# Optimization experiments

Hardware: AMD Instinct MI355X
Metric: run time of the kernel (lower is better)

## Reference

```python
import jax, jax.numpy as jnp
import numpy as np

N, L, C, H = 8, 2048, 512, 512
C_HALF = max(C // 2, 1)


def setup_inputs() -> dict:
    key = jax.random.key(0)
    ks = jax.random.split(key, 11)
    s = 0.02
    return {
        "x": jax.random.normal(ks[0], (N, L, C), dtype=jnp.float32),
        "theta_w": jax.random.normal(ks[1], (C, H), dtype=jnp.float32) * s,
        "theta_b": jax.random.normal(ks[2], (H,), dtype=jnp.float32) * s,
        "phi_w": jax.random.normal(ks[3], (C, H), dtype=jnp.float32) * s,
        "phi_b": jax.random.normal(ks[4], (H,), dtype=jnp.float32) * s,
        "psi_w": jax.random.normal(ks[5], (C, H), dtype=jnp.float32) * s,
        "psi_b": jax.random.normal(ks[6], (H,), dtype=jnp.float32) * s,
        "r1_w": jax.random.normal(ks[7], (H, C_HALF), dtype=jnp.float32) * s,
        "r1_b": jax.random.normal(ks[8], (C_HALF,), dtype=jnp.float32) * s,
        "r2_w": jax.random.normal(ks[9], (C_HALF, C), dtype=jnp.float32) * s,
        "r2_b": jax.random.normal(ks[10], (C,), dtype=jnp.float32) * s,
    }


def reference(x, theta_w, theta_b, phi_w, phi_b, psi_w, psi_b, r1_w, r1_b, r2_w, r2_b):
    # projections: [n, L, h]
    x_t = x @ theta_w + theta_b
    x_ph = x @ phi_w + phi_b
    x_psi = x @ psi_w + psi_b
    # unscaled attention: phi @ theta^T -> [n, L, L], softmax over last dim
    attn = jax.nn.softmax(jnp.einsum("nlh,nmh->nlm", x_ph, x_t), axis=2)
    x_add = jnp.einsum("nlm,nmh->nlh", attn, x_psi)
    # recover MLP with LeakyReLU(0.2) then Tanh, residual add
    h1 = jax.nn.leaky_relu(x_add @ r1_w + r1_b, negative_slope=0.2)
    h2 = jnp.tanh(h1 @ r2_w + r2_b)
    return x + h2
```

## Files before the change

kernel.cpp:

```cpp
#include <hip/hip_runtime.h>
#include <hip/hip_bf16.h>

typedef float f32x4 __attribute__((ext_vector_type(4)));
typedef int   v8i   __attribute__((ext_vector_type(8)));
typedef __attribute__((address_space(3))) unsigned int       lds_uint;
typedef __attribute__((address_space(1))) const unsigned int glb_uint;

__device__ __forceinline__ float tanh_fast(float x) {
    float e = __expf(-2.0f * fabsf(x));
    float r = (1.0f - e) / (1.0f + e);
    return copysignf(r, x);
}
__device__ __forceinline__ unsigned char f2fp8(float v) {
    return (unsigned char)(__builtin_amdgcn_cvt_pk_fp8_f32(v, 0.0f, 0, false) & 0xff);
}
__device__ __forceinline__ unsigned short f2h(float v) {
    _Float16 h = (_Float16)v;
    unsigned short u;
    __builtin_memcpy(&u, &h, 2);
    return u;
}
__device__ __forceinline__ float h2f(unsigned short u) {
    _Float16 h;
    __builtin_memcpy(&h, &u, 2);
    return (float)h;
}

__global__ __launch_bounds__(256) void prep(
    const float* __restrict__ x,
    const float* __restrict__ theta_w, const float* __restrict__ phi_w,
    const float* __restrict__ psi_w,   const float* __restrict__ r1_w,
    const float* __restrict__ r2_w,
    const float* __restrict__ theta_b, const float* __restrict__ phi_b,
    const float* __restrict__ psi_b,
    unsigned char* __restrict__ xb8, unsigned char* __restrict__ wCat8T,
    unsigned char* __restrict__ r1T8, unsigned char* __restrict__ r2T8,
    float* __restrict__ bCat) {
    const int b = blockIdx.x, t = threadIdx.x;
    if (b < 8192) {
        long i = ((long)b * 256 + t) * 4;
        float4 f = *(const float4*)(x + i);
        int w = __builtin_amdgcn_cvt_pk_fp8_f32(f.x, f.y, 0, false);
        w = __builtin_amdgcn_cvt_pk_fp8_f32(f.z, f.w, w, true);
        *(unsigned int*)(xb8 + i) = (unsigned int)w;
    } else if (b < 11264) {
        const int sel = (b - 8192) >> 10;
        const int idx = ((b - 8192) & 1023) * 256 + t;
        const float* w = sel == 0 ? theta_w : (sel == 1 ? phi_w : psi_w);
        const int r = idx >> 9, c = idx & 511;
        wCat8T[(long)(sel * 512 + c) * 512 + r] = f2fp8(w[idx] * 16.0f);
    } else if (b < 11776) {
        const int idx = (b - 11264) * 256 + t;
        const int r = idx >> 8, c = idx & 255;
        r1T8[(long)c * 512 + r] = f2fp8(r1_w[idx] * 16.0f);
    } else if (b < 12288) {
        const int idx = (b - 11776) * 256 + t;
        const int r = idx >> 9, c = idx & 511;
        r2T8[(long)c * 256 + r] = f2fp8(r2_w[idx] * 16.0f);
    } else {
        const int i = (b - 12288) * 256 + t;
        if (i < 1536)
            bCat[i] = i < 512 ? theta_b[i] : (i < 1024 ? phi_b[i - 512] : psi_b[i - 1024]);
    }
}

__global__ __launch_bounds__(256) void softmax_fp8(unsigned short* __restrict__ S) {
    const size_t row = (size_t)blockIdx.y * 2048 + blockIdx.x;
    unsigned short* p = S + row * 2048;
    const int t = threadIdx.x;
    uint4 raw = *(uint4*)(p + t * 8);
    unsigned int w[4] = {raw.x, raw.y, raw.z, raw.w};
    float v[8];
#pragma unroll
    for (int i = 0; i < 4; ++i) {
        v[2 * i]     = h2f((unsigned short)(w[i] & 0xffffu));
        v[2 * i + 1] = h2f((unsigned short)(w[i] >> 16));
    }
    float mx = v[0];
#pragma unroll
    for (int i = 1; i < 8; ++i) mx = fmaxf(mx, v[i]);
#pragma unroll
    for (int off = 32; off > 0; off >>= 1) mx = fmaxf(mx, __shfl_xor(mx, off));
    __shared__ float red[8];
    const int wave = t >> 6, lane = t & 63;
    if (lane == 0) red[wave] = mx;
    __syncthreads();
    mx = fmaxf(fmaxf(red[0], red[1]), fmaxf(red[2], red[3]));
    float s = 0.0f;
#pragma unroll
    for (int i = 0; i < 8; ++i) { v[i] = __expf(v[i] - mx); s += v[i]; }
#pragma unroll
    for (int off = 32; off > 0; off >>= 1) s += __shfl_xor(s, off);
    if (lane == 0) red[4 + wave] = s;
    __syncthreads();
    s = red[4] + red[5] + red[6] + red[7];
    const float inv = 1.0f / s;
    int o0 = __builtin_amdgcn_cvt_pk_fp8_f32(v[0] * inv, v[1] * inv, 0, false);
    o0 = __builtin_amdgcn_cvt_pk_fp8_f32(v[2] * inv, v[3] * inv, o0, true);
    int o1 = __builtin_amdgcn_cvt_pk_fp8_f32(v[4] * inv, v[5] * inv, 0, false);
    o1 = __builtin_amdgcn_cvt_pk_fp8_f32(v[6] * inv, v[7] * inv, o1, true);
    uint2 ov; ov.x = (unsigned int)o0; ov.y = (unsigned int)o1;
    *(uint2*)((unsigned char*)p + t * 8) = ov;
}

template <int MODE>
__global__ __launch_bounds__(256) void gemm_fp8(
    const unsigned char* __restrict__ A,
    const unsigned char* __restrict__ Bt,
    const float* __restrict__ bias,
    const float* __restrict__ resid,
    unsigned short* __restrict__ outH,
    unsigned char* __restrict__ out8,
    unsigned char* __restrict__ out8b,
    unsigned char* __restrict__ outV,
    float* __restrict__ outF,
    int K, int ldaB, int ldbB, int ldc, long sA, long sB, long sC) {
    __shared__ unsigned char As[2][128 * 128];
    __shared__ unsigned char Bs[2][128 * 128];

    const int tid  = threadIdx.x;
    const int lane = tid & 63, wave = tid >> 6;
    const int m16  = lane & 15, quad = lane >> 4;
    const int wm   = (wave >> 1) << 6, wn = (wave & 1) << 6;

    int bx, by, z;
    if constexpr (MODE == 1) {
        z = blockIdx.x & 7;
        const int t = blockIdx.x >> 3;
        by = t & 15; bx = t >> 4;
    } else if constexpr (MODE == 2) {
        z = blockIdx.x & 7;
        const int t = blockIdx.x >> 3;
        by = t & 3;  bx = t >> 2;
    } else {
        bx = blockIdx.x; by = blockIdx.y; z = 0;
    }
    const int m0 = bx << 7, n0 = by << 7;

    const int srow = lane >> 3;
    const int uswz = (lane & 7) ^ srow;

    const unsigned char* Abase = A  + (long)z * sA + (long)m0 * ldaB;
    const unsigned char* Bbase = Bt + (long)z * sB + (long)n0 * ldbB;
    const int stR = (wave << 5) + srow;
    const long gA0 = (long)stR * ldaB + (uswz << 4);
    const long gB0 = (long)stR * ldbB + (uswz << 4);

    const int s8  = m16 & 7;
    const int P   = quad ^ (s8 >> 1);
    const int cLo = (P << 1) + (s8 & 1);
    const int offLo = cLo << 4;
    const int offHi = (cLo ^ 1) << 4;

    f32x4 acc[4][4] = {};
    union F8 { v8i v; int4 q[2]; };

    auto STAGE = [&](int buf, int kk) {
#pragma unroll
        for (int i = 0; i < 4; ++i) {
            const unsigned char* gp = Abase + gA0 + (long)(i << 3) * ldaB + kk;
            unsigned char* lp = &As[buf][((wave << 5) + (i << 3)) << 7];
            __builtin_amdgcn_global_load_lds((glb_uint*)gp, (lds_uint*)lp, 16, 0, 0);
        }
#pragma unroll
        for (int i = 0; i < 4; ++i) {
            const unsigned char* gp = Bbase + gB0 + (long)(i << 3) * ldbB + kk;
            unsigned char* lp = &Bs[buf][((wave << 5) + (i << 3)) << 7];
            __builtin_amdgcn_global_load_lds((glb_uint*)gp, (lds_uint*)lp, 16, 0, 0);
        }
    };

    STAGE(0, 0);
    int cur = 0;
    for (int k0 = 0; k0 < K; k0 += 128) {
        if (k0 + 128 < K) {
            STAGE(cur ^ 1, k0 + 128);
            asm volatile("s_waitcnt vmcnt(8)" ::: "memory");
        } else {
            asm volatile("s_waitcnt vmcnt(0)" ::: "memory");
        }
        asm volatile("s_barrier" ::: "memory");

        const unsigned char* Ab = As[cur];
        const unsigned char* Bb = Bs[cur];
        F8 af[4], bg[4];
#pragma unroll
        for (int f = 0; f < 4; ++f) {
            const int m = wm + (f << 4) + m16;
            const int n = wn + (f << 4) + m16;
            af[f].q[0] = *(const int4*)&Ab[(m << 7) + offLo];
            af[f].q[1] = *(const int4*)&Ab[(m << 7) + offHi];
            bg[f].q[0] = *(const int4*)&Bb[(n << 7) + offLo];
            bg[f].q[1] = *(const int4*)&Bb[(n << 7) + offHi];
        }
#pragma unroll
        for (int fi = 0; fi < 4; ++fi)
#pragma unroll
            for (int fj = 0; fj < 4; ++fj)
                acc[fi][fj] = __builtin_amdgcn_mfma_scale_f32_16x16x128_f8f6f4(
                    af[fi].v, bg[fj].v, acc[fi][fj],
                    0, 0, 0, 127, 0, 127);

        asm volatile("s_waitcnt lgkmcnt(0)" ::: "memory");
        asm volatile("s_barrier" ::: "memory");
        cur ^= 1;
    }

    const long zC = (long)z * sC;

    if (MODE == 0) {
        const int sel = n0 >> 9;
        if (sel < 2) {
            unsigned char* dst = sel == 0 ? out8 : out8b;
#pragma unroll
            for (int fj = 0; fj < 4; ++fj) {
                const int col = n0 + wn + (fj << 4) + m16;
                const int cb  = col & 511;
                const float bv = bias[col];
#pragma unroll
                for (int fi = 0; fi < 4; ++fi)
#pragma unroll
                    for (int r = 0; r < 4; ++r) {
                        const int row = m0 + wm + (fi << 4) + (quad << 2) + r;
                        dst[(long)row * 512 + cb] = f2fp8(acc[fi][fj][r] * 0.0625f + bv);
                    }
            }
        } else {
            const int zz = m0 >> 11, l0 = (m0 & 2047) + wm + (quad << 2);
#pragma unroll
            for (int fj = 0; fj < 4; ++fj) {
                const int col = n0 + wn + (fj << 4) + m16;
                const int h   = col & 511;
                const float bv = bias[col];
#pragma unroll
                for (int fi = 0; fi < 4; ++fi) {
                    int w = __builtin_amdgcn_cvt_pk_fp8_f32(
                        acc[fi][fj][0] * 0.0625f + bv, acc[fi][fj][1] * 0.0625f + bv, 0, false);
                    w = __builtin_amdgcn_cvt_pk_fp8_f32(
                        acc[fi][fj][2] * 0.0625f + bv, acc[fi][fj][3] * 0.0625f + bv, w, true);
                    *(unsigned int*)(outV + ((long)zz * 512 + h) * 2048 + l0 + (fi << 4)) =
                        (unsigned int)w;
                }
            }
        }
    } else {
#pragma unroll
        for (int fj = 0; fj < 4; ++fj) {
            const int col = n0 + wn + (fj << 4) + m16;
            float bv = 0.0f;
            if (MODE >= 3) bv = bias[col];
#pragma unroll
            for (int fi = 0; fi < 4; ++fi)
#pragma unroll
                for (int r = 0; r < 4; ++r) {
                    const int row = m0 + wm + (fi << 4) + (quad << 2) + r;
                    float v = acc[fi][fj][r];
                    if (MODE == 1) {
                        outH[zC + (long)row * ldc + col] = f2h(v);
                    } else if (MODE == 2) {
                        out8[zC + (long)row * 512 + col] = f2fp8(v);
                    } else if (MODE == 3) {
                        v = v * 0.0625f + bv;
                        v = v > 0.0f ? v : 0.2f * v;
                        out8[(long)row * 256 + col] = f2fp8(v);
                    } else {
                        v = v * 0.0625f + bv;
                        const long idx = (long)row * ldc + col;
                        outF[idx] = tanh_fast(v) + resid[idx];
                    }
                }
        }
    }
}

extern "C" void kernel_launch(void* const* d_in, const int* in_sizes, int n_in,
                              void* d_out, int out_size, void* d_ws, size_t ws_size,
                              hipStream_t stream) {
    const float* x       = (const float*)d_in[0];
    const float* theta_w = (const float*)d_in[1];
    const float* theta_b = (const float*)d_in[2];
    const float* phi_w   = (const float*)d_in[3];
    const float* phi_b   = (const float*)d_in[4];
    const float* psi_w   = (const float*)d_in[5];
    const float* psi_b   = (const float*)d_in[6];
    const float* r1_w    = (const float*)d_in[7];
    const float* r1_b    = (const float*)d_in[8];
    const float* r2_w    = (const float*)d_in[9];
    const float* r2_b    = (const float*)d_in[10];
    float* out = (float*)d_out;

    constexpr int  N = 8, L = 2048, C = 512, H = 512, CH = 256;
    constexpr long NL = (long)N * L;

    char* p = (char*)d_ws;
    auto alloc = [&](size_t bytes) { void* q = (void*)p; p += bytes; return q; };
    unsigned char*  xb8    = (unsigned char*)alloc(NL * C);
    unsigned char*  TH8    = (unsigned char*)alloc(NL * H);
    unsigned char*  PH8    = (unsigned char*)alloc(NL * H);
    unsigned char*  VT8    = (unsigned char*)alloc((long)N * H * L);
    unsigned char*  xadd8  = (unsigned char*)alloc(NL * H);
    unsigned char*  h18    = (unsigned char*)alloc(NL * CH);
    unsigned char*  wCat8T = (unsigned char*)alloc((long)1536 * 512);
    unsigned char*  r1T8   = (unsigned char*)alloc((long)H * CH);
    unsigned char*  r2T8   = (unsigned char*)alloc((long)CH * C);
    float*          bCat   = (float*)alloc(1536 * 4 + 256);
    unsigned short* S      = (unsigned short*)alloc((long)N * L * L * 2);

    prep<<<12294, 256, 0, stream>>>(x, theta_w, phi_w, psi_w, r1_w, r2_w,
                                    theta_b, phi_b, psi_b, xb8, wCat8T, r1T8, r2T8, bCat);

    gemm_fp8<0><<<dim3(NL / 128, 1536 / 128, 1), 256, 0, stream>>>(
        xb8, wCat8T, bCat, nullptr, nullptr, TH8, PH8, VT8, nullptr,
        C, C, C, 0, 0, 0, 0);

    gemm_fp8<1><<<dim3((L / 128) * (L / 128) * N, 1, 1), 256, 0, stream>>>(
        PH8, TH8, nullptr, nullptr, S, nullptr, nullptr, nullptr, nullptr,
        H, H, H, L, (long)L * H, (long)L * H, (long)L * L);

    softmax_fp8<<<dim3(L, N), 256, 0, stream>>>(S);

    gemm_fp8<2><<<dim3((L / 128) * (H / 128) * N, 1, 1), 256, 0, stream>>>(
        (const unsigned char*)S, VT8, nullptr, nullptr, nullptr, xadd8, nullptr, nullptr, nullptr,
        L, 2 * L, L, H, (long)L * 2 * L, (long)H * L, (long)L * H);

    gemm_fp8<3><<<dim3(NL / 128, CH / 128, 1), 256, 0, stream>>>(
        xadd8, r1T8, r1_b, nullptr, nullptr, h18, nullptr, nullptr, nullptr,
        H, H, H, CH, 0, 0, 0);

    gemm_fp8<4><<<dim3(NL / 128, C / 128, 1), 256, 0, stream>>>(
        h18, r2T8, r2_b, x, nullptr, nullptr, nullptr, nullptr, out,
        CH, CH, CH, C, 0, 0, 0);
}
```

Baseline: 220.7 us.

## Stage GEMM epilogues through swizzled LDS for coalesced 16-byte stores, remap MODE0 blocks

The fp8/fp16 outputs of modes 0-3 were written as scattered byte or short stores per accumulator element. They are now staged into the A shared-memory buffer with an XOR swizzle, then written back as 16-byte rows by each thread pair, so global writes coalesce. The projection GEMM also moves to a 1D grid with a remapped block order meant to improve cache locality. The cost is an extra LDS round trip and a barrier per block.

```diff
diff --git a/kernel.cpp b/kernel.cpp
--- a/kernel.cpp
+++ b/kernel.cpp
@@ -124,7 +124,13 @@
     const int wm   = (wave >> 1) << 6, wn = (wave & 1) << 6;
 
     int bx, by, z;
-    if constexpr (MODE == 1) {
+    if constexpr (MODE == 0) {
+        z = 0;
+        const int x = blockIdx.x & 7;
+        const int t = blockIdx.x >> 3;
+        bx = x * 16 + t / 12;
+        by = t % 12;
+    } else if constexpr (MODE == 1) {
         z = blockIdx.x & 7;
         const int t = blockIdx.x >> 3;
         by = t & 15; bx = t >> 4;
@@ -207,23 +213,35 @@
     }
 
     const long zC = (long)z * sC;
+    unsigned char* Cs = &As[0][0];
 
     if (MODE == 0) {
         const int sel = n0 >> 9;
         if (sel < 2) {
+#pragma unroll
+            for (int fj = 0; fj < 4; ++fj) {
+                const int ct = wn + (fj << 4) + m16;
+                const int u  = ct >> 4, lo = ct & 15;
+                const float bv = bias[n0 + ct];
+#pragma unroll
+                for (int fi = 0; fi < 4; ++fi)
+#pragma unroll
+                    for (int r = 0; r < 4; ++r) {
+                        const int row = wm + (fi << 4) + (quad << 2) + r;
+                        Cs[row * 128 + ((u ^ (row & 7)) << 4) + lo] =
+                            f2fp8(acc[fi][fj][r] * 0.0625f + bv);
+                    }
+            }
+            asm volatile("s_waitcnt lgkmcnt(0)" ::: "memory");
+            asm volatile("s_barrier" ::: "memory");
             unsigned char* dst = sel == 0 ? out8 : out8b;
-#pragma unroll
-            for (int fj = 0; fj < 4; ++fj) {
-                const int col = n0 + wn + (fj << 4) + m16;
-                const int cb  = col & 511;
-                const float bv = bias[col];
-#pragma unroll
-                for (int fi = 0; fi < 4; ++fi)
-#pragma unroll
-                    for (int r = 0; r < 4; ++r) {
-                        const int row = m0 + wm + (fi << 4) + (quad << 2) + r;
-                        dst[(long)row * 512 + cb] = f2fp8(acc[fi][fj][r] * 0.0625f + bv);
-                    }
+            const int row = tid >> 1, p2 = tid & 1;
+            const long gb = (long)(m0 + row) * 512 + (n0 & 511);
+#pragma unroll
+            for (int j = 0; j < 4; ++j) {
+                const int u = (p2 << 2) + j;
+                uint4 v = *(const uint4*)(Cs + row * 128 + ((u ^ (row & 7)) << 4));
+                *(uint4*)(dst + gb + (u << 4)) = v;
             }
         } else {
             const int zz = m0 >> 11, l0 = (m0 & 2047) + wm + (quad << 2);
@@ -243,31 +261,74 @@
                 }
             }
         }
+    } else if (MODE == 1) {
+#pragma unroll
+        for (int fj = 0; fj < 4; ++fj) {
+            const int ct = wn + (fj << 4) + m16;
+            const int u  = ct >> 3, lo = (ct & 7) << 1;
+#pragma unroll
+            for (int fi = 0; fi < 4; ++fi)
+#pragma unroll
+                for (int r = 0; r < 4; ++r) {
+                    const int row = wm + (fi << 4) + (quad << 2) + r;
+                    *(unsigned short*)(Cs + row * 256 + ((u ^ (row & 7)) << 4) + lo) =
+                        f2h(acc[fi][fj][r]);
+                }
+        }
+        asm volatile("s_waitcnt lgkmcnt(0)" ::: "memory");
+        asm volatile("s_barrier" ::: "memory");
+        const int row = tid >> 1, p2 = tid & 1;
+        const long gb = zC + (long)(m0 + row) * ldc + n0;
+#pragma unroll
+        for (int j = 0; j < 8; ++j) {
+            const int u = (p2 << 3) + j;
+            uint4 v = *(const uint4*)(Cs + row * 256 + ((u ^ (row & 7)) << 4));
+            *(uint4*)(outH + gb + (u << 3)) = v;
+        }
+    } else if (MODE == 2 || MODE == 3) {
+#pragma unroll
+        for (int fj = 0; fj < 4; ++fj) {
+            const int ct = wn + (fj << 4) + m16;
+            const int u  = ct >> 4, lo = ct & 15;
+            float bv = 0.0f;
+            if (MODE == 3) bv = bias[n0 + ct];
+#pragma unroll
+            for (int fi = 0; fi < 4; ++fi)
+#pragma unroll
+                for (int r = 0; r < 4; ++r) {
+                    const int row = wm + (fi << 4) + (quad << 2) + r;
+                    float v = acc[fi][fj][r];
+                    if (MODE == 3) {
+                        v = v * 0.0625f + bv;
+                        v = v > 0.0f ? v : 0.2f * v;
+                    }
+                    Cs[row * 128 + ((u ^ (row & 7)) << 4) + lo] = f2fp8(v);
+                }
+        }
+        asm volatile("s_waitcnt lgkmcnt(0)" ::: "memory");
+        asm volatile("s_barrier" ::: "memory");
+        const int row = tid >> 1, p2 = tid & 1;
+        const int pitch = (MODE == 2) ? 512 : 256;
+        const long gb = (MODE == 2 ? zC : 0) + (long)(m0 + row) * pitch + n0;
+#pragma unroll
+        for (int j = 0; j < 4; ++j) {
+            const int u = (p2 << 2) + j;
+            uint4 v = *(const uint4*)(Cs + row * 128 + ((u ^ (row & 7)) << 4));
+            *(uint4*)(out8 + gb + (u << 4)) = v;
+        }
     } else {
 #pragma unroll
         for (int fj = 0; fj < 4; ++fj) {
             const int col = n0 + wn + (fj << 4) + m16;
-            float bv = 0.0f;
-            if (MODE >= 3) bv = bias[col];
+            const float bv = bias[col];
 #pragma unroll
             for (int fi = 0; fi < 4; ++fi)
 #pragma unroll
                 for (int r = 0; r < 4; ++r) {
                     const int row = m0 + wm + (fi << 4) + (quad << 2) + r;
-                    float v = acc[fi][fj][r];
-                    if (MODE == 1) {
-                        outH[zC + (long)row * ldc + col] = f2h(v);
-                    } else if (MODE == 2) {
-                        out8[zC + (long)row * 512 + col] = f2fp8(v);
-                    } else if (MODE == 3) {
-                        v = v * 0.0625f + bv;
-                        v = v > 0.0f ? v : 0.2f * v;
-                        out8[(long)row * 256 + col] = f2fp8(v);
-                    } else {
-                        v = v * 0.0625f + bv;
-                        const long idx = (long)row * ldc + col;
-                        outF[idx] = tanh_fast(v) + resid[idx];
-                    }
+                    float v = acc[fi][fj][r] * 0.0625f + bv;
+                    const long idx = (long)row * ldc + col;
+                    outF[idx] = tanh_fast(v) + resid[idx];
                 }
         }
     }
@@ -309,7 +370,7 @@
     prep<<<12294, 256, 0, stream>>>(x, theta_w, phi_w, psi_w, r1_w, r2_w,
                                     theta_b, phi_b, psi_b, xb8, wCat8T, r1T8, r2T8, bCat);
 
-    gemm_fp8<0><<<dim3(NL / 128, 1536 / 128, 1), 256, 0, stream>>>(
+    gemm_fp8<0><<<dim3((NL / 128) * (1536 / 128), 1, 1), 256, 0, stream>>>(
         xb8, wCat8T, bCat, nullptr, nullptr, TH8, PH8, VT8, nullptr,
         C, C, C, 0, 0, 0, 0);
 
```

Result: slower. 240.3 us (+8.9%).
